# Kernel optimization log

Measured on AMD Instinct MI355X. Metric: run time of the kernel, lower is better.

The kernel has to match this reference:

```python
import jax, jax.numpy as jnp
import numpy as np

D_MODEL = 2048
D_FF = 8192
BATCH = 4
SEQ = 2048
MAX_EXP = 4
NUM_BITS = 8
C_CHUNKS = 2
SCALE = 0.1


def _pow2_ternary(key, out_dim, in_dim, max_exp):
    """Weights are t * 2^{-e}: ternary sign times power-of-two magnitude."""
    k1, k2 = jax.random.split(key)
    t = jax.random.randint(k1, (out_dim, in_dim), -1, 2).astype(jnp.float32)
    e = jax.random.randint(k2, (out_dim, in_dim), 0, max_exp + 1).astype(jnp.float32)
    return t * jnp.exp2(-e)


def setup_inputs() -> dict:
    key = jax.random.key(0)
    kx, k1, k2 = jax.random.split(key, 3)
    x = jax.random.normal(kx, (BATCH, SEQ, D_MODEL), dtype=jnp.float32)
    W1 = _pow2_ternary(k1, D_FF, D_MODEL, MAX_EXP)   # [d_ff, d_model] torch-style
    W2 = _pow2_ternary(k2, D_MODEL, D_FF, MAX_EXP)   # [d_model, d_ff]
    return {"x": x, "W1": W1, "W2": W2}


def _lookup_act(h):
    # 16-bit (num_bits * c) fixed-point quantize, then table-valued GELU.
    total_bits = NUM_BITS * C_CHUNKS
    qmax = 2 ** (total_bits - 1) - 1
    qmin = -(2 ** (total_bits - 1))
    q = jnp.clip(jnp.round(h / SCALE), qmin, qmax)
    return jax.nn.gelu(q * SCALE)


def reference(x, W1, W2):
    # fc1: [b,s,d_model] x [d_ff,d_model]^T -> [b,s,d_ff]
    h = jnp.einsum('bsd,fd->bsf', x, W1)
    a = _lookup_act(h)
    # fc2: [b,s,d_ff] x [d_model,d_ff]^T -> [b,s,d_model]
    return jnp.einsum('bsf,df->bsd', a, W2)
```

## Files before the change

### kernel.cpp

```cpp
#include <hip/hip_runtime.h>
#include <cstdint>
#include <cstddef>


typedef __bf16 bf16_t;
typedef bf16_t bf16x8 __attribute__((ext_vector_type(8)));
typedef float  floatx4 __attribute__((ext_vector_type(4)));

#define AS1 __attribute__((address_space(1)))
#define AS3 __attribute__((address_space(3)))

__device__ __forceinline__ void async_cp16(const void* g, void* l) {
    __builtin_amdgcn_global_load_lds((const AS1 void*)g, (AS3 void*)l, 16, 0, 0);
}

__device__ __forceinline__ float gelu_fast(float x) {
    const float C0 = 1.5957691216057308f;
    const float C1 = 0.0713548163f;
    float u2 = x * fmaf(C1, x * x, C0);
    float e  = __expf(u2);
    float r  = __builtin_amdgcn_rcpf(1.0f + e);
    return x * (1.0f - r);
}

__global__ __launch_bounds__(256)
void cvt_pack_swz(const float* __restrict__ src, bf16_t* __restrict__ dst,
                  int K, int tshift)
{
    const size_t   oc = (size_t)blockIdx.x * 256 + threadIdx.x;
    const uint32_t ho = ((uint32_t)oc & 1023u) * 16u;
    const size_t   region = oc >> 10;
    const int      h  = (int)(region & 1);
    const size_t   pt = region >> 1;
    const int      t  = (int)(pt & ((1u << tshift) - 1));
    const size_t   p  = pt >> tshift;
    const uint32_t L = ho ^ (((ho >> 9) & 1u) << 5);
    const int      s = (int)(L >> 10);
    const uint32_t u = L & 1023u;
    const size_t   row = p * 256 + (size_t)(h * 128 + (s >> 1) * 16 + (int)(u >> 6));
    const int      k   = (t << 6) + (s & 1) * 32 + (int)((u & 63u) >> 1);
    const float* sp = src + row * (size_t)K + k;
    float4 a = *(const float4*)sp;
    float4 b = *(const float4*)(sp + 4);
    bf16x8 o;
    o[0] = (bf16_t)a.x; o[1] = (bf16_t)a.y; o[2] = (bf16_t)a.z; o[3] = (bf16_t)a.w;
    o[4] = (bf16_t)b.x; o[5] = (bf16_t)b.y; o[6] = (bf16_t)b.z; o[7] = (bf16_t)b.w;
    *(bf16x8*)(dst + oc * 8) = o;
}

template<bool ACT, typename OutT>
__global__ __launch_bounds__(512, 2)
void gemm256(const bf16_t* __restrict__ A, const bf16_t* __restrict__ B,
             OutT* __restrict__ C, int M, int N, int K, int nbxs)
{
    __shared__ __align__(16) bf16_t lds[65536];
    char* const ldsb = (char*)lds;

    const int NT  = K >> 6;
    const int id  = blockIdx.x;
    const int nwg = gridDim.x;
    const int sw = (id & 7) * (nwg >> 3) + (id >> 3);
    const int by = sw >> nbxs;
    const int bx = sw & ((1 << nbxs) - 1);

    const int tid  = threadIdx.x;
    const int lane = tid & 63;
    const int wave = tid >> 6;
    const int wm = wave >> 2;
    const int wn = wave & 3;

    const bf16_t* const Ap = A + (size_t)by * NT * 16384;
    const bf16_t* const Bp = B + (size_t)bx * NT * 16384;

    uint32_t lsw = (uint32_t)(((lane & 15) << 6) + ((lane >> 4) << 4));
    lsw ^= ((lsw >> 9) & 1u) << 5;

    const uint32_t aBase = (uint32_t)(2 + wm) << 14;
    const uint32_t bBase = (uint32_t)(wn >> 1) << 14;
    const int bSub = (wn & 1) * 4;

    floatx4 acc[8][4];
    #pragma unroll
    for (int i = 0; i < 8; ++i)
      #pragma unroll
      for (int j = 0; j < 4; ++j)
        acc[i][j] = (floatx4)0.0f;

    auto stage = [&](int t, int j) {
        const bf16_t* g = (j < 2) ? (Bp + (size_t)t * 16384 + (size_t)j * 8192)
                                  : (Ap + (size_t)t * 16384 + (size_t)(j - 2) * 8192);
        char* l = ldsb + (((t & 1) << 16) + (j << 14));
        async_cp16((const char*)g + tid * 16, l + tid * 16);
        async_cp16((const char*)g + 8192 + tid * 16, l + 8192 + tid * 16);
    };

    stage(0, 0); stage(0, 1); stage(0, 2); stage(0, 3);
    stage(1, 0); stage(1, 1); stage(1, 2); stage(1, 3);
    asm volatile("s_waitcnt vmcnt(8)" ::: "memory");
    __builtin_amdgcn_s_barrier();

    bf16x8 b01[2][2];
    {
        const char* bB0 = ldsb + bBase;
        #pragma unroll
        for (int fn = 0; fn < 2; ++fn)
          #pragma unroll
          for (int ks = 0; ks < 2; ++ks)
            b01[fn][ks] = *(const bf16x8*)(bB0 + (((((bSub + fn) << 1) + ks) << 10) | lsw));
    }

    for (int t = 0; t < NT; ++t) {
        const char* aB  = ldsb + ((t & 1) << 16) + aBase;
        const char* bBc = ldsb + ((t & 1) << 16) + bBase;
        const bool s1 = (t + 1 < NT);
        const bool s2 = (t + 2 < NT);

        bf16x8 af[4][2], b23[2][2];
        #pragma unroll
        for (int fm = 0; fm < 4; ++fm)
          #pragma unroll
          for (int ks = 0; ks < 2; ++ks)
            af[fm][ks] = *(const bf16x8*)(aB + ((((fm << 1) + ks) << 10) | lsw));
        #pragma unroll
        for (int fn = 0; fn < 2; ++fn)
          #pragma unroll
          for (int ks = 0; ks < 2; ++ks)
            b23[fn][ks] = *(const bf16x8*)(bBc + (((((bSub + 2 + fn) << 1) + ks) << 10) | lsw));
        __builtin_amdgcn_s_setprio(1);
        #pragma unroll
        for (int ks = 0; ks < 2; ++ks)
          #pragma unroll
          for (int fm = 0; fm < 4; ++fm)
            #pragma unroll
            for (int fn = 0; fn < 2; ++fn)
              acc[fm][fn] = __builtin_amdgcn_mfma_f32_16x16x32_bf16(
                  af[fm][ks], b01[fn][ks], acc[fm][fn], 0, 0, 0);
        __builtin_amdgcn_s_setprio(0);

        asm volatile("s_waitcnt lgkmcnt(0)" ::: "memory");
        __builtin_amdgcn_s_barrier();
        if (s2) { stage(t + 2, 0); stage(t + 2, 1); }
        __builtin_amdgcn_s_setprio(1);
        #pragma unroll
        for (int ks = 0; ks < 2; ++ks)
          #pragma unroll
          for (int fm = 0; fm < 4; ++fm)
            #pragma unroll
            for (int fn = 0; fn < 2; ++fn)
              acc[fm][2 + fn] = __builtin_amdgcn_mfma_f32_16x16x32_bf16(
                  af[fm][ks], b23[fn][ks], acc[fm][2 + fn], 0, 0, 0);
        __builtin_amdgcn_s_setprio(0);

        bf16x8 ah[4][2];
        #pragma unroll
        for (int fm = 0; fm < 4; ++fm)
          #pragma unroll
          for (int ks = 0; ks < 2; ++ks)
            ah[fm][ks] = *(const bf16x8*)(aB + (((((4 + fm) << 1) + ks) << 10) | lsw));
        __builtin_amdgcn_s_setprio(1);
        #pragma unroll
        for (int ks = 0; ks < 2; ++ks)
          #pragma unroll
          for (int fm = 0; fm < 4; ++fm)
            #pragma unroll
            for (int fn = 0; fn < 2; ++fn)
              acc[4 + fm][fn] = __builtin_amdgcn_mfma_f32_16x16x32_bf16(
                  ah[fm][ks], b01[fn][ks], acc[4 + fm][fn], 0, 0, 0);
        __builtin_amdgcn_s_setprio(0);

        if (s2)      asm volatile("s_waitcnt vmcnt(4)" ::: "memory");
        else if (s1) asm volatile("s_waitcnt vmcnt(0)" ::: "memory");
        __builtin_amdgcn_s_barrier();
        if (s1) {
            const char* bBn = ldsb + (((t + 1) & 1) << 16) + bBase;
            #pragma unroll
            for (int fn = 0; fn < 2; ++fn)
              #pragma unroll
              for (int ks = 0; ks < 2; ++ks)
                b01[fn][ks] = *(const bf16x8*)(bBn + (((((bSub + fn) << 1) + ks) << 10) | lsw));
        }
        if (s2) { stage(t + 2, 2); stage(t + 2, 3); }
        __builtin_amdgcn_s_setprio(1);
        #pragma unroll
        for (int ks = 0; ks < 2; ++ks)
          #pragma unroll
          for (int fm = 0; fm < 4; ++fm)
            #pragma unroll
            for (int fn = 0; fn < 2; ++fn)
              acc[4 + fm][2 + fn] = __builtin_amdgcn_mfma_f32_16x16x32_bf16(
                  ah[fm][ks], b23[fn][ks], acc[4 + fm][2 + fn], 0, 0, 0);
        __builtin_amdgcn_s_setprio(0);
    }

    if constexpr (ACT) {
        __syncthreads();
        const uint32_t rbase = (uint32_t)(wn * 2 + wm) << 14;
        #pragma unroll
        for (int fm = 0; fm < 8; ++fm)
          #pragma unroll
          for (int fn = 0; fn < 4; ++fn)
            #pragma unroll
            for (int r = 0; r < 4; ++r) {
                float h = acc[fm][fn][r];
                float q = rintf(h * 10.0f);
                q = fminf(fmaxf(q, -32768.0f), 32767.0f);
                h = gelu_fast(q * 0.1f);
                uint32_t L = ((uint32_t)((fm << 1) + (fn >> 1)) << 10)
                           + (uint32_t)((((lane >> 4) << 2) + r) << 6)
                           + (uint32_t)((((fn & 1) << 4) + (lane & 15)) << 1);
                uint32_t P = L ^ (((L >> 9) & 1u) << 5);
                *(bf16_t*)(ldsb + rbase + P) = (bf16_t)h;
            }
        __syncthreads();
        const int nkt2 = N >> 6;
        bf16_t* const Cb = (bf16_t*)C;
        #pragma unroll
        for (int it = 0; it < 16; ++it) {
            const int ch = it * 512 + tid;
            const int rg = ch >> 10;
            const int c  = ch & 1023;
            const size_t gr = ((size_t)by * nkt2 + (size_t)(bx * 4) + (rg >> 1)) * 2
                            + (size_t)(rg & 1);
            bf16x8 v = *(const bf16x8*)(ldsb + (size_t)ch * 16);
            *(bf16x8*)((char*)Cb + gr * 16384 + (size_t)c * 16) = v;
        }
    } else {
        const int r0 = by * 256 + wm * 128;
        const int c0 = bx * 256 + wn * 64;
        #pragma unroll
        for (int fm = 0; fm < 8; ++fm)
          #pragma unroll
          for (int fn = 0; fn < 4; ++fn) {
            const int col = c0 + fn * 16 + (lane & 15);
            #pragma unroll
            for (int r = 0; r < 4; ++r) {
              const int row = r0 + fm * 16 + ((lane >> 4) << 2) + r;
              C[(size_t)row * N + col] = (OutT)acc[fm][fn][r];
            }
          }
    }
}

extern "C" void kernel_launch(void* const* d_in, const int* in_sizes, int n_in,
                              void* d_out, int out_size, void* d_ws, size_t ws_size,
                              hipStream_t stream)
{
    const int M  = 8192;
    const int DM = 2048;
    const int DF = 8192;

    const float* x  = (const float*)d_in[0];
    const float* W1 = (const float*)d_in[1];
    const float* W2 = (const float*)d_in[2];
    float* out = (float*)d_out;

    bf16_t* xb  = (bf16_t*)d_ws;
    bf16_t* w1b = xb  + (size_t)M  * DM;
    bf16_t* w2b = w1b + (size_t)DF * DM;
    bf16_t* act = w2b + (size_t)DM * DF;

    cvt_pack_swz<<<8192, 256, 0, stream>>>(x,  xb,  DM, 5);
    cvt_pack_swz<<<8192, 256, 0, stream>>>(W1, w1b, DM, 5);
    cvt_pack_swz<<<8192, 256, 0, stream>>>(W2, w2b, DF, 7);

    gemm256<true, bf16_t><<<dim3(1024), 512, 0, stream>>>(xb, w1b, act, M, DF, DM, 5);
    gemm256<false, float><<<dim3(256), 512, 0, stream>>>(act, w2b, out, M, DM, DF, 3);
}
```

Before: 638.0 us.

## Restructure GEMM main loop into ping-pong tile phases with explicit barriers

Replaces the software-pipelined K loop with a lambda processing one tile per call, unrolled twice so the LDS buffer selector is a compile-time constant. Each tile is split into four MFMA phases separated by workgroup barriers and sched_barriers, with LDS fragment reads issued just before each phase rather than prefetched across iterations. The aim is a ping-pong style schedule in which waves interleave memory and MFMA work, with cheaper address arithmetic. The cost is many more barriers per tile and the loss of the cross-iteration b01 prefetch. The loop also assumes NT is even.

```diff
diff --git a/kernel.cpp b/kernel.cpp
--- a/kernel.cpp
+++ b/kernel.cpp
@@ -75,8 +75,8 @@
     uint32_t lsw = (uint32_t)(((lane & 15) << 6) + ((lane >> 4) << 4));
     lsw ^= ((lsw >> 9) & 1u) << 5;
 
-    const uint32_t aBase = (uint32_t)(2 + wm) << 14;
-    const uint32_t bBase = (uint32_t)(wn >> 1) << 14;
+    const uint32_t aOff = (uint32_t)(2 + wm) << 14;
+    const uint32_t bOff = (uint32_t)(wn >> 1) << 14;
     const int bSub = (wn & 1) * 4;
 
     floatx4 acc[8][4];
@@ -86,110 +86,113 @@
       for (int j = 0; j < 4; ++j)
         acc[i][j] = (floatx4)0.0f;
 
-    auto stage = [&](int t, int j) {
+    auto stage = [&](int t, int j, int bsel) {
         const bf16_t* g = (j < 2) ? (Bp + (size_t)t * 16384 + (size_t)j * 8192)
                                   : (Ap + (size_t)t * 16384 + (size_t)(j - 2) * 8192);
-        char* l = ldsb + (((t & 1) << 16) + (j << 14));
+        char* l = ldsb + ((bsel << 16) + (j << 14));
         async_cp16((const char*)g + tid * 16, l + tid * 16);
         async_cp16((const char*)g + 8192 + tid * 16, l + 8192 + tid * 16);
     };
 
-    stage(0, 0); stage(0, 1); stage(0, 2); stage(0, 3);
-    stage(1, 0); stage(1, 1); stage(1, 2); stage(1, 3);
+    auto tile = [&](int t, int bsel) {
+        const char* aB = ldsb + (bsel << 16) + aOff;
+        const char* bB = ldsb + (bsel << 16) + bOff;
+        const bool s2 = (t + 2 < NT);
+        bf16x8 af[4][2], ah[4][2], b01[2][2], b23[2][2];
+
+        #pragma unroll
+        for (int fm = 0; fm < 4; ++fm)
+          #pragma unroll
+          for (int ks = 0; ks < 2; ++ks)
+            af[fm][ks] = *(const bf16x8*)(aB + ((((fm << 1) + ks) << 10) | lsw));
+        #pragma unroll
+        for (int fn = 0; fn < 2; ++fn)
+          #pragma unroll
+          for (int ks = 0; ks < 2; ++ks)
+            b01[fn][ks] = *(const bf16x8*)(bB + (((((bSub + fn) << 1) + ks) << 10) | lsw));
+        asm volatile("s_waitcnt lgkmcnt(8)" ::: "memory");
+        __builtin_amdgcn_s_barrier();
+        asm volatile("s_waitcnt lgkmcnt(0)" ::: "memory");
+        __builtin_amdgcn_sched_barrier(0);
+        __builtin_amdgcn_s_setprio(1);
+        #pragma unroll
+        for (int ks = 0; ks < 2; ++ks)
+          #pragma unroll
+          for (int fm = 0; fm < 4; ++fm)
+            #pragma unroll
+            for (int fn = 0; fn < 2; ++fn)
+              acc[fm][fn] = __builtin_amdgcn_mfma_f32_16x16x32_bf16(
+                  af[fm][ks], b01[fn][ks], acc[fm][fn], 0, 0, 0);
+        __builtin_amdgcn_s_setprio(0);
+        __builtin_amdgcn_s_barrier();
+
+        #pragma unroll
+        for (int fn = 0; fn < 2; ++fn)
+          #pragma unroll
+          for (int ks = 0; ks < 2; ++ks)
+            b23[fn][ks] = *(const bf16x8*)(bB + (((((bSub + 2 + fn) << 1) + ks) << 10) | lsw));
+        __builtin_amdgcn_s_barrier();
+        asm volatile("s_waitcnt lgkmcnt(0)" ::: "memory");
+        __builtin_amdgcn_sched_barrier(0);
+        __builtin_amdgcn_s_setprio(1);
+        #pragma unroll
+        for (int ks = 0; ks < 2; ++ks)
+          #pragma unroll
+          for (int fm = 0; fm < 4; ++fm)
+            #pragma unroll
+            for (int fn = 0; fn < 2; ++fn)
+              acc[fm][2 + fn] = __builtin_amdgcn_mfma_f32_16x16x32_bf16(
+                  af[fm][ks], b23[fn][ks], acc[fm][2 + fn], 0, 0, 0);
+        __builtin_amdgcn_s_setprio(0);
+        __builtin_amdgcn_s_barrier();
+
+        #pragma unroll
+        for (int fm = 0; fm < 4; ++fm)
+          #pragma unroll
+          for (int ks = 0; ks < 2; ++ks)
+            ah[fm][ks] = *(const bf16x8*)(aB + (((((4 + fm) << 1) + ks) << 10) | lsw));
+        if (s2) { stage(t + 2, 0, bsel); stage(t + 2, 1, bsel); }
+        __builtin_amdgcn_s_barrier();
+        asm volatile("s_waitcnt lgkmcnt(0)" ::: "memory");
+        __builtin_amdgcn_sched_barrier(0);
+        __builtin_amdgcn_s_setprio(1);
+        #pragma unroll
+        for (int ks = 0; ks < 2; ++ks)
+          #pragma unroll
+          for (int fm = 0; fm < 4; ++fm)
+            #pragma unroll
+            for (int fn = 0; fn < 2; ++fn)
+              acc[4 + fm][fn] = __builtin_amdgcn_mfma_f32_16x16x32_bf16(
+                  ah[fm][ks], b01[fn][ks], acc[4 + fm][fn], 0, 0, 0);
+        __builtin_amdgcn_s_setprio(0);
+        __builtin_amdgcn_s_barrier();
+
+        if (s2) { stage(t + 2, 2, bsel); stage(t + 2, 3, bsel); }
+        if (s2) asm volatile("s_waitcnt vmcnt(8)" ::: "memory");
+        else    asm volatile("s_waitcnt vmcnt(0)" ::: "memory");
+        __builtin_amdgcn_s_barrier();
+        __builtin_amdgcn_sched_barrier(0);
+        __builtin_amdgcn_s_setprio(1);
+        #pragma unroll
+        for (int ks = 0; ks < 2; ++ks)
+          #pragma unroll
+          for (int fm = 0; fm < 4; ++fm)
+            #pragma unroll
+            for (int fn = 0; fn < 2; ++fn)
+              acc[4 + fm][2 + fn] = __builtin_amdgcn_mfma_f32_16x16x32_bf16(
+                  ah[fm][ks], b23[fn][ks], acc[4 + fm][2 + fn], 0, 0, 0);
+        __builtin_amdgcn_s_setprio(0);
+        __builtin_amdgcn_s_barrier();
+    };
+
+    stage(0, 0, 0); stage(0, 1, 0); stage(0, 2, 0); stage(0, 3, 0);
+    stage(1, 0, 1); stage(1, 1, 1); stage(1, 2, 1); stage(1, 3, 1);
     asm volatile("s_waitcnt vmcnt(8)" ::: "memory");
     __builtin_amdgcn_s_barrier();
 
-    bf16x8 b01[2][2];
-    {
-        const char* bB0 = ldsb + bBase;
-        #pragma unroll
-        for (int fn = 0; fn < 2; ++fn)
-          #pragma unroll
-          for (int ks = 0; ks < 2; ++ks)
-            b01[fn][ks] = *(const bf16x8*)(bB0 + (((((bSub + fn) << 1) + ks) << 10) | lsw));
-    }
-
-    for (int t = 0; t < NT; ++t) {
-        const char* aB  = ldsb + ((t & 1) << 16) + aBase;
-        const char* bBc = ldsb + ((t & 1) << 16) + bBase;
-        const bool s1 = (t + 1 < NT);
-        const bool s2 = (t + 2 < NT);
-
-        bf16x8 af[4][2], b23[2][2];
-        #pragma unroll
-        for (int fm = 0; fm < 4; ++fm)
-          #pragma unroll
-          for (int ks = 0; ks < 2; ++ks)
-            af[fm][ks] = *(const bf16x8*)(aB + ((((fm << 1) + ks) << 10) | lsw));
-        #pragma unroll
-        for (int fn = 0; fn < 2; ++fn)
-          #pragma unroll
-          for (int ks = 0; ks < 2; ++ks)
-            b23[fn][ks] = *(const bf16x8*)(bBc + (((((bSub + 2 + fn) << 1) + ks) << 10) | lsw));
-        __builtin_amdgcn_s_setprio(1);
-        #pragma unroll
-        for (int ks = 0; ks < 2; ++ks)
-          #pragma unroll
-          for (int fm = 0; fm < 4; ++fm)
-            #pragma unroll
-            for (int fn = 0; fn < 2; ++fn)
-              acc[fm][fn] = __builtin_amdgcn_mfma_f32_16x16x32_bf16(
-                  af[fm][ks], b01[fn][ks], acc[fm][fn], 0, 0, 0);
-        __builtin_amdgcn_s_setprio(0);
-
-        asm volatile("s_waitcnt lgkmcnt(0)" ::: "memory");
-        __builtin_amdgcn_s_barrier();
-        if (s2) { stage(t + 2, 0); stage(t + 2, 1); }
-        __builtin_amdgcn_s_setprio(1);
-        #pragma unroll
-        for (int ks = 0; ks < 2; ++ks)
-          #pragma unroll
-          for (int fm = 0; fm < 4; ++fm)
-            #pragma unroll
-            for (int fn = 0; fn < 2; ++fn)
-              acc[fm][2 + fn] = __builtin_amdgcn_mfma_f32_16x16x32_bf16(
-                  af[fm][ks], b23[fn][ks], acc[fm][2 + fn], 0, 0, 0);
-        __builtin_amdgcn_s_setprio(0);
-
-        bf16x8 ah[4][2];
-        #pragma unroll
-        for (int fm = 0; fm < 4; ++fm)
-          #pragma unroll
-          for (int ks = 0; ks < 2; ++ks)
-            ah[fm][ks] = *(const bf16x8*)(aB + (((((4 + fm) << 1) + ks) << 10) | lsw));
-        __builtin_amdgcn_s_setprio(1);
-        #pragma unroll
-        for (int ks = 0; ks < 2; ++ks)
-          #pragma unroll
-          for (int fm = 0; fm < 4; ++fm)
-            #pragma unroll
-            for (int fn = 0; fn < 2; ++fn)
-              acc[4 + fm][fn] = __builtin_amdgcn_mfma_f32_16x16x32_bf16(
-                  ah[fm][ks], b01[fn][ks], acc[4 + fm][fn], 0, 0, 0);
-        __builtin_amdgcn_s_setprio(0);
-
-        if (s2)      asm volatile("s_waitcnt vmcnt(4)" ::: "memory");
-        else if (s1) asm volatile("s_waitcnt vmcnt(0)" ::: "memory");
-        __builtin_amdgcn_s_barrier();
-        if (s1) {
-            const char* bBn = ldsb + (((t + 1) & 1) << 16) + bBase;
-            #pragma unroll
-            for (int fn = 0; fn < 2; ++fn)
-              #pragma unroll
-              for (int ks = 0; ks < 2; ++ks)
-                b01[fn][ks] = *(const bf16x8*)(bBn + (((((bSub + fn) << 1) + ks) << 10) | lsw));
-        }
-        if (s2) { stage(t + 2, 2); stage(t + 2, 3); }
-        __builtin_amdgcn_s_setprio(1);
-        #pragma unroll
-        for (int ks = 0; ks < 2; ++ks)
-          #pragma unroll
-          for (int fm = 0; fm < 4; ++fm)
-            #pragma unroll
-            for (int fn = 0; fn < 2; ++fn)
-              acc[4 + fm][2 + fn] = __builtin_amdgcn_mfma_f32_16x16x32_bf16(
-                  ah[fm][ks], b23[fn][ks], acc[4 + fm][2 + fn], 0, 0, 0);
-        __builtin_amdgcn_s_setprio(0);
+    for (int tp = 0; tp < NT; tp += 2) {
+        tile(tp, 0);
+        tile(tp + 1, 1);
     }
 
     if constexpr (ACT) {
```

New measurement: 683.8 us. +7.2%, slower.
